# Performance work log

Hardware: AMD Instinct MI355X
Metric: run time of the kernel (lower is better)

The kernel has to match this reference:

```python
import jax, jax.numpy as jnp
import numpy as np

D_MODEL = 1024


def setup_inputs() -> dict:
    key = jax.random.key(0)
    ks = jax.random.split(key, 11)
    B, Sq, Skv, D = 16, 2048, 2048, D_MODEL
    s = 1.0 / np.sqrt(D)
    return {
        "q": jax.random.normal(ks[0], (B, Sq, D), jnp.float32),
        "k": jax.random.normal(ks[1], (B, Skv, D), jnp.float32),
        "v": jax.random.normal(ks[2], (B, Skv, D), jnp.float32),
        "Wq": jax.random.normal(ks[3], (D, D), jnp.float32) * s,
        "bq": jnp.zeros((D,), jnp.float32),
        "Wk": jax.random.normal(ks[4], (D, D), jnp.float32) * s,
        "bk": jnp.zeros((D,), jnp.float32),
        "Wv": jax.random.normal(ks[5], (D, D), jnp.float32) * s,
        "bv": jnp.zeros((D,), jnp.float32),
        "Wo": jax.random.normal(ks[6], (D, D), jnp.float32) * s,
        "bo": jnp.zeros((D,), jnp.float32),
    }


def reference(q, k, v, Wq, bq, Wk, bk, Wv, bv, Wo, bo):
    D = q.shape[-1]
    # Projections (torch Linear: x @ W^T + b; here W stored as [in, out])
    query = q @ Wq + bq          # [B, Sq, D]
    key_p = k @ Wk + bk          # [B, Skv, D]
    value = v @ Wv + bv          # [B, Skv, D]
    # Scaled dot-product attention, scale by sqrt(d_model) (single head)
    scores = jnp.einsum('bqd,bkd->bqk', query / jnp.sqrt(jnp.float32(D)), key_p)
    attn = jax.nn.softmax(scores, axis=-1)   # dropout p=0.0 -> identity
    out = jnp.einsum('bqk,bkd->bqd', attn, value)
    return out @ Wo + bo
```

## Files before the change

### kernel.cpp

```cpp
#include <hip/hip_runtime.h>

typedef unsigned int u32;
typedef unsigned short u16;
typedef __attribute__((ext_vector_type(8))) __bf16 bf16x8;
typedef __attribute__((ext_vector_type(4))) float f32x4;

typedef __attribute__((address_space(1))) void as1_void;
typedef __attribute__((address_space(3))) void as3_void;

__device__ __forceinline__ u16 f2bf(float f){
  u32 u = __builtin_bit_cast(u32, f);
  return (u16)((u + 0x7FFFu + ((u >> 16) & 1u)) >> 16);
}
__device__ __forceinline__ float bf2f(u16 h){
  u32 u = ((u32)h) << 16;
  return __builtin_bit_cast(float, u);
}

__device__ __forceinline__ void gload16(const void* g, void* l){
  __builtin_amdgcn_global_load_lds((as1_void*)(unsigned long long)g, (as3_void*)l, 16, 0, 0);
}
__device__ __forceinline__ bf16x8 ldfrag(const char* p){
  return __builtin_bit_cast(bf16x8, *(const uint4*)p);
}

__global__ void wcast(const float* __restrict__ W, float scale, u16* __restrict__ out){
  __shared__ float t[32][33];
  int bx = blockIdx.x * 32, by = blockIdx.y * 32;
  int tx = threadIdx.x, ty = threadIdx.y;
  #pragma unroll
  for (int i = 0; i < 32; i += 8) t[ty + i][tx] = W[(size_t)(bx + ty + i) * 1024 + by + tx];
  __syncthreads();
  #pragma unroll
  for (int i = 0; i < 32; i += 8)
    out[(size_t)(by + ty + i) * 1024 + bx + tx] = f2bf(scale * t[tx][ty + i]);
}

__global__ __launch_bounds__(256) void castbf(const float* __restrict__ in, u16* __restrict__ out, int n8){
  int stride = gridDim.x * blockDim.x;
  for (int i = blockIdx.x * blockDim.x + threadIdx.x; i < n8; i += stride){
    const float4* p = (const float4*)(in + (size_t)i * 8);
    float4 f0 = p[0], f1 = p[1];
    union { uint4 u; u16 h[8]; } uu;
    uu.h[0]=f2bf(f0.x); uu.h[1]=f2bf(f0.y); uu.h[2]=f2bf(f0.z); uu.h[3]=f2bf(f0.w);
    uu.h[4]=f2bf(f1.x); uu.h[5]=f2bf(f1.y); uu.h[6]=f2bf(f1.z); uu.h[7]=f2bf(f1.w);
    ((uint4*)out)[i] = uu.u;
  }
}

__global__ __launch_bounds__(256) void softmax_rows(u16* __restrict__ S){
  __shared__ float red[8];
  size_t row = blockIdx.x;
  uint4* p = (uint4*)(S + row * 2048);
  int tid = threadIdx.x;
  int lane = tid & 63, wave = tid >> 6;
  union { uint4 u4; u16 h[8]; } uu;
  uu.u4 = p[tid];
  float v[8];
  float m = -1e30f;
  #pragma unroll
  for (int j = 0; j < 8; j++){ v[j] = bf2f(uu.h[j]); m = fmaxf(m, v[j]); }
  #pragma unroll
  for (int o = 32; o; o >>= 1) m = fmaxf(m, __shfl_xor(m, o));
  if (lane == 0) red[wave] = m;
  __syncthreads();
  m = fmaxf(fmaxf(red[0], red[1]), fmaxf(red[2], red[3]));
  float s = 0.f;
  #pragma unroll
  for (int j = 0; j < 8; j++){ v[j] = __expf(v[j] - m); s += v[j]; }
  #pragma unroll
  for (int o = 32; o; o >>= 1) s += __shfl_xor(s, o);
  if (lane == 0) red[4 + wave] = s;
  __syncthreads();
  s = red[4] + red[5] + red[6] + red[7];
  float inv = 1.f / s;
  #pragma unroll
  for (int j = 0; j < 8; j++) uu.h[j] = f2bf(v[j] * inv);
  p[tid] = uu.u4;
}


template<int MO, int N0>
__device__ __forceinline__ void phase_mfma(f32x4 (&acc)[8][4], bf16x8 (&a)[4][2], bf16x8 (&b)[4][2]){
  __builtin_amdgcn_s_setprio(1);
  #pragma unroll
  for (int ks = 0; ks < 2; ks++)
    #pragma unroll
    for (int mm = 0; mm < 4; mm++)
      #pragma unroll
      for (int nn = 0; nn < 2; nn++)
        acc[MO + mm][N0 + nn] = __builtin_amdgcn_mfma_f32_16x16x32_bf16(
            a[mm][ks], b[N0 + nn][ks], acc[MO + mm][N0 + nn], 0, 0, 0);
  __builtin_amdgcn_s_setprio(0);
}

template<int BIAS, int OUTF32>
__global__ __launch_bounds__(512, 2) void gemm8(
    const u16* __restrict__ A, const u16* __restrict__ B, void* __restrict__ C,
    const float* __restrict__ bias, float bscale, int K,
    long long sA, long long sB, long long sC,
    int lda, int ldb, int ldc, int gx, int gxy)
{
  __shared__ u16 sm[2][2][16384];
  char* smb = (char*)&sm[0][0][0];

  int tid = threadIdx.x;
  int lane = tid & 63, wave = tid >> 6;
  int wr = wave >> 2, wc = wave & 3;
  int l15 = lane & 15, l4 = lane >> 4;

  int nwg = gxy * gridDim.z;
  int lin = blockIdx.x + gx * blockIdx.y + gxy * blockIdx.z;
  int cpx = nwg >> 3;
  int swz = (lin & 7) * cpx + (lin >> 3);
  int tz = swz / gxy; int rem = swz - tz * gxy;
  int ty = rem / gx;  int tx = rem - ty * gx;
  long long zb = tz;
  int row0 = tx * 256, col0 = ty * 256;

  const char* Aglob = (const char*)(A + zb * sA + (size_t)row0 * lda);
  const char* Bglob = (const char*)(B + zb * sB + (size_t)col0 * ldb);

  int r = tid >> 3, cl = tid & 7;
  int ldsb = r * 128 + cl * 16;
  u32 aoff[4], boff[4];
  #pragma unroll
  for (int i = 0; i < 4; i++){
    int row = i * 64 + r;
    int ksw = (cl ^ (r & 7)) * 8;
    aoff[i] = (u32)(((u32)row * (u32)lda + (u32)ksw) * 2u);
    boff[i] = (u32)(((u32)row * (u32)ldb + (u32)ksw) * 2u);
  }
  u32 ardo[2], brdo[2];
  #pragma unroll
  for (int ks = 0; ks < 2; ks++){
    u32 sw = (u32)(((ks * 4 + l4) ^ (l15 & 7)) * 16);
    ardo[ks] = (u32)(wr * 16384 + l15 * 128) + sw;
    brdo[ks] = (u32)(wc * 8192 + l15 * 128) + sw;
  }

#define STA(i, tau, bb) gload16(Aglob + aoff[i] + (size_t)(tau) * 128, smb + (bb) * 65536 + (i) * 8192 + ldsb)
#define STB(i, tau, bb) gload16(Bglob + boff[i] + (size_t)(tau) * 128, smb + (bb) * 65536 + 32768 + (i) * 8192 + ldsb)

  int NT = K >> 6;

  STA(0, 0, 0); STA(2, 0, 0);
  STB(0, 0, 0); STB(1, 0, 0);
  STB(2, 0, 0); STB(3, 0, 0);
  STA(1, 0, 0); STA(3, 0, 0);
  STA(0, 1, 1); STA(2, 1, 1);
  STB(0, 1, 1); STB(1, 1, 1);
  STB(2, 1, 1); STB(3, 1, 1);
  asm volatile("s_waitcnt vmcnt(6)" ::: "memory");
  __builtin_amdgcn_s_barrier();

  f32x4 acc[8][4] = {};
  bf16x8 a[4][2], b[4][2];

  for (int t = 0; t < NT; t++){
    int cur = t & 1;
    const char* Abase = smb + cur * 65536;
    const char* Bbase = Abase + 32768;

    #pragma unroll
    for (int mm = 0; mm < 4; mm++)
      #pragma unroll
      for (int ks = 0; ks < 2; ks++)
        a[mm][ks] = ldfrag(Abase + mm * 2048 + ardo[ks]);
    #pragma unroll
    for (int nn = 0; nn < 2; nn++)
      #pragma unroll
      for (int ks = 0; ks < 2; ks++)
        b[nn][ks] = ldfrag(Bbase + nn * 2048 + brdo[ks]);
    if (t + 1 < NT){ STA(1, t + 1, cur ^ 1); STA(3, t + 1, cur ^ 1); }
    __builtin_amdgcn_s_barrier();
    phase_mfma<0, 0>(acc, a, b);
    __builtin_amdgcn_s_barrier();

    #pragma unroll
    for (int nn = 2; nn < 4; nn++)
      #pragma unroll
      for (int ks = 0; ks < 2; ks++)
        b[nn][ks] = ldfrag(Bbase + nn * 2048 + brdo[ks]);
    if (t + 2 < NT){ STA(0, t + 2, cur); STA(2, t + 2, cur); }
    __builtin_amdgcn_s_barrier();
    phase_mfma<0, 2>(acc, a, b);
    __builtin_amdgcn_s_barrier();

    #pragma unroll
    for (int mm = 0; mm < 4; mm++)
      #pragma unroll
      for (int ks = 0; ks < 2; ks++)
        a[mm][ks] = ldfrag(Abase + (4 + mm) * 2048 + ardo[ks]);
    if (t + 2 < NT){ STB(0, t + 2, cur); STB(1, t + 2, cur); }
    __builtin_amdgcn_s_barrier();
    phase_mfma<4, 0>(acc, a, b);
    __builtin_amdgcn_s_barrier();

    if (t + 2 < NT){ STB(2, t + 2, cur); STB(3, t + 2, cur); }
    if (t < NT - 2) asm volatile("s_waitcnt vmcnt(6)" ::: "memory");
    else            asm volatile("s_waitcnt vmcnt(0)" ::: "memory");
    __builtin_amdgcn_s_barrier();
    phase_mfma<4, 2>(acc, a, b);
    __builtin_amdgcn_s_barrier();
  }
#undef STA
#undef STB

  #pragma unroll
  for (int m = 0; m < 8; m++){
    #pragma unroll
    for (int n = 0; n < 4; n++){
      int gr0 = row0 + wr * 128 + m * 16 + l4 * 4;
      int gc  = col0 + wc * 64 + n * 16 + l15;
      float bcol = (BIAS == 1) ? bscale * bias[gc] : 0.f;
      #pragma unroll
      for (int j = 0; j < 4; j++){
        float vv = acc[m][n][j];
        int gr = gr0 + j;
        if (BIAS == 1) vv += bcol;
        if (BIAS == 2) vv += bscale * bias[gr];
        if (OUTF32) ((float*)C)[zb * sC + (size_t)gr * ldc + gc] = vv;
        else        ((u16*) C)[zb * sC + (size_t)gr * ldc + gc] = f2bf(vv);
      }
    }
  }
}

extern "C" void kernel_launch(void* const* d_in, const int* in_sizes, int n_in,
                              void* d_out, int out_size, void* d_ws, size_t ws_size,
                              hipStream_t stream){
  const float* q  = (const float*)d_in[0];
  const float* k  = (const float*)d_in[1];
  const float* v  = (const float*)d_in[2];
  const float* Wq = (const float*)d_in[3];
  const float* bq = (const float*)d_in[4];
  const float* Wk = (const float*)d_in[5];
  const float* bk = (const float*)d_in[6];
  const float* Wv = (const float*)d_in[7];
  const float* bv = (const float*)d_in[8];
  const float* Wo = (const float*)d_in[9];
  const float* bo = (const float*)d_in[10];

  char* ws = (char*)d_ws;
  const size_t MB = (size_t)1 << 20;
  u16* Wqt = (u16*)(ws + 0 * MB);
  u16* Wkt = (u16*)(ws + 2 * MB);
  u16* Wvt = (u16*)(ws + 4 * MB);
  u16* Wot = (u16*)(ws + 6 * MB);
  u16* Qp  = (u16*)(ws + 8 * MB);
  u16* Kp  = (u16*)(ws + 72 * MB);
  u16* Vt  = (u16*)(ws + 136 * MB);
  u16* S   = (u16*)(ws + 200 * MB);
  u16* O   = (u16*)(ws + 328 * MB);
  u16* X   = (u16*)(ws + 200 * MB);
  float* out = (float*)d_out;

  dim3 wb(32, 8);
  wcast<<<dim3(32, 32), wb, 0, stream>>>(Wq, 1.f / 32.f, Wqt);
  wcast<<<dim3(32, 32), wb, 0, stream>>>(Wk, 1.f, Wkt);
  wcast<<<dim3(32, 32), wb, 0, stream>>>(Wv, 1.f, Wvt);
  wcast<<<dim3(32, 32), wb, 0, stream>>>(Wo, 1.f, Wot);

  const int n8 = 16 * 2048 * 1024 / 8;

  castbf<<<dim3(2048), 256, 0, stream>>>(q, X, n8);
  gemm8<1,0><<<dim3(128, 4, 1), 512, 0, stream>>>(X, Wqt, Qp, bq, 1.f/32.f,
      1024, 0, 0, 0, 1024, 1024, 1024, 128, 512);
  castbf<<<dim3(2048), 256, 0, stream>>>(k, X, n8);
  gemm8<1,0><<<dim3(128, 4, 1), 512, 0, stream>>>(X, Wkt, Kp, bk, 1.f,
      1024, 0, 0, 0, 1024, 1024, 1024, 128, 512);
  castbf<<<dim3(2048), 256, 0, stream>>>(v, X, n8);
  gemm8<2,0><<<dim3(4, 8, 16), 512, 0, stream>>>(Wvt, X, Vt, bv, 1.f,
      1024, 0, 2048LL * 1024, 1024LL * 2048, 1024, 1024, 2048, 4, 32);
  gemm8<0,0><<<dim3(8, 8, 16), 512, 0, stream>>>(Qp, Kp, S, nullptr, 0.f,
      1024, 2048LL * 1024, 2048LL * 1024, 2048LL * 2048, 1024, 1024, 2048, 8, 64);
  softmax_rows<<<dim3(32768), 256, 0, stream>>>(S);
  gemm8<0,0><<<dim3(8, 4, 16), 512, 0, stream>>>(S, Vt, O, nullptr, 0.f,
      2048, 2048LL * 2048, 1024LL * 2048, 2048LL * 1024, 2048, 2048, 1024, 8, 32);
  gemm8<1,1><<<dim3(128, 4, 1), 512, 0, stream>>>(O, Wot, out, bo, 1.f,
      1024, 0, 0, 0, 1024, 1024, 1024, 128, 512);
}
```

Measured before the change: 727.3 us.

## Make GEMM persistent over multiple tiles with cross-tile prefetch pipelining

The GEMM kernel now launches a fixed 256 workgroups, each processing TPB consecutive output tiles. The global-to-LDS prefetch pipeline continues across tile boundaries, so the ramp-up and drain of the double buffer overlap with the next tile and the tail wave is removed. The value bias is moved from the V projection, where it was a row bias, into the attention-times-V GEMM as a column bias. This relies on softmax rows summing to one. The tile-to-workgroup mapping assumes tile counts are multiples of 256*TPB, which adds complexity and register pressure.

```diff
diff --git a/kernel.cpp b/kernel.cpp
--- a/kernel.cpp
+++ b/kernel.cpp
@@ -97,29 +97,20 @@
 template<int BIAS, int OUTF32>
 __global__ __launch_bounds__(512, 2) void gemm8(
     const u16* __restrict__ A, const u16* __restrict__ B, void* __restrict__ C,
-    const float* __restrict__ bias, float bscale, int K,
+    const float* __restrict__ bias, float bscale, int NT,
     long long sA, long long sB, long long sC,
-    int lda, int ldb, int ldc, int gx, int gxy)
+    int lda, int ldb, int ldc, int gx, int gxy, int TPB)
 {
   __shared__ u16 sm[2][2][16384];
-  char* smb = (char*)&sm[0][0][0];
+  char* smb = (char*)sm;
 
   int tid = threadIdx.x;
   int lane = tid & 63, wave = tid >> 6;
   int wr = wave >> 2, wc = wave & 3;
   int l15 = lane & 15, l4 = lane >> 4;
 
-  int nwg = gxy * gridDim.z;
-  int lin = blockIdx.x + gx * blockIdx.y + gxy * blockIdx.z;
-  int cpx = nwg >> 3;
-  int swz = (lin & 7) * cpx + (lin >> 3);
-  int tz = swz / gxy; int rem = swz - tz * gxy;
-  int ty = rem / gx;  int tx = rem - ty * gx;
-  long long zb = tz;
-  int row0 = tx * 256, col0 = ty * 256;
-
-  const char* Aglob = (const char*)(A + zb * sA + (size_t)row0 * lda);
-  const char* Bglob = (const char*)(B + zb * sB + (size_t)col0 * ldb);
+  int b = blockIdx.x;
+  int lin0 = ((b & 7) * 32 + (b >> 3)) * TPB;
 
   int r = tid >> 3, cl = tid & 7;
   int ldsb = r * 128 + cl * 16;
@@ -139,92 +130,129 @@
     brdo[ks] = (u32)(wc * 8192 + l15 * 128) + sw;
   }
 
-#define STA(i, tau, bb) gload16(Aglob + aoff[i] + (size_t)(tau) * 128, smb + (bb) * 65536 + (i) * 8192 + ldsb)
-#define STB(i, tau, bb) gload16(Bglob + boff[i] + (size_t)(tau) * 128, smb + (bb) * 65536 + 32768 + (i) * 8192 + ldsb)
-
-  int NT = K >> 6;
-
-  STA(0, 0, 0); STA(2, 0, 0);
-  STB(0, 0, 0); STB(1, 0, 0);
-  STB(2, 0, 0); STB(3, 0, 0);
-  STA(1, 0, 0); STA(3, 0, 0);
-  STA(0, 1, 1); STA(2, 1, 1);
-  STB(0, 1, 1); STB(1, 1, 1);
-  STB(2, 1, 1); STB(3, 1, 1);
+  auto tcoord = [&](int lin, int& x, int& y, int& z){
+    z = lin / gxy; int rem = lin - z * gxy; y = rem / gx; x = rem - y * gx;
+  };
+  auto abase = [&](int lin){ int x, y, z; tcoord(lin, x, y, z);
+    return (const char*)(A + (long long)z * sA + (size_t)(x * 256) * lda); };
+  auto bbase = [&](int lin){ int x, y, z; tcoord(lin, x, y, z);
+    return (const char*)(B + (long long)z * sB + (size_t)(y * 256) * ldb); };
+
+  int tx, ty, tz;
+  tcoord(lin0, tx, ty, tz);
+  int row0 = tx * 256, col0 = ty * 256;
+  long long zbC = tz;
+
+  float bc0[4], bc1[4];
+  if (BIAS){
+    int xx, yy, zz;
+    tcoord(lin0, xx, yy, zz);
+    int c0 = yy * 256 + wc * 64 + l15;
+    #pragma unroll
+    for (int n = 0; n < 4; n++) bc0[n] = bscale * bias[c0 + n * 16];
+    tcoord(lin0 + (TPB > 1 ? 1 : 0), xx, yy, zz);
+    c0 = yy * 256 + wc * 64 + l15;
+    #pragma unroll
+    for (int n = 0; n < 4; n++) bc1[n] = bscale * bias[c0 + n * 16];
+  }
+
+  const char* AgM = abase(lin0);
+  const char* AgP = AgM;
+  const char* BgP = bbase(lin0);
+  int km = 1, kp = 2, jm = 0, jp = 0, kk = 0, jj = 0;
+
+#define STA(bse, i, kq, bb) gload16((bse) + aoff[i] + (size_t)(kq) * 128, smb + (bb) * 65536 + (i) * 8192 + ldsb)
+#define STB(bse, i, kq, bb) gload16((bse) + boff[i] + (size_t)(kq) * 128, smb + (bb) * 65536 + 32768 + (i) * 8192 + ldsb)
+
+  STA(AgM, 0, 0, 0); STA(AgM, 2, 0, 0);
+  STB(BgP, 0, 0, 0); STB(BgP, 1, 0, 0); STB(BgP, 2, 0, 0); STB(BgP, 3, 0, 0);
+  STA(AgM, 1, 0, 0); STA(AgM, 3, 0, 0);
+  STA(AgM, 0, 1, 1); STA(AgM, 2, 1, 1);
+  STB(BgP, 0, 1, 1); STB(BgP, 1, 1, 1); STB(BgP, 2, 1, 1); STB(BgP, 3, 1, 1);
   asm volatile("s_waitcnt vmcnt(6)" ::: "memory");
   __builtin_amdgcn_s_barrier();
 
   f32x4 acc[8][4] = {};
-  bf16x8 a[4][2], b[4][2];
-
-  for (int t = 0; t < NT; t++){
-    int cur = t & 1;
-    const char* Abase = smb + cur * 65536;
-    const char* Bbase = Abase + 32768;
+  bf16x8 a[4][2], bfr[4][2];
+  int S = TPB * NT;
+
+  for (int s = 0; s < S; s++){
+    int cur = s & 1;
+    const char* Ab = smb + cur * 65536;
+    const char* Bb = Ab + 32768;
+    bool st1 = (s + 1 < S), st2 = (s + 2 < S);
 
     #pragma unroll
     for (int mm = 0; mm < 4; mm++)
       #pragma unroll
       for (int ks = 0; ks < 2; ks++)
-        a[mm][ks] = ldfrag(Abase + mm * 2048 + ardo[ks]);
+        a[mm][ks] = ldfrag(Ab + mm * 2048 + ardo[ks]);
     #pragma unroll
     for (int nn = 0; nn < 2; nn++)
       #pragma unroll
       for (int ks = 0; ks < 2; ks++)
-        b[nn][ks] = ldfrag(Bbase + nn * 2048 + brdo[ks]);
-    if (t + 1 < NT){ STA(1, t + 1, cur ^ 1); STA(3, t + 1, cur ^ 1); }
-    __builtin_amdgcn_s_barrier();
-    phase_mfma<0, 0>(acc, a, b);
+        bfr[nn][ks] = ldfrag(Bb + nn * 2048 + brdo[ks]);
+    if (st1){ STA(AgM, 1, km, cur ^ 1); STA(AgM, 3, km, cur ^ 1); }
+    __builtin_amdgcn_s_barrier();
+    phase_mfma<0, 0>(acc, a, bfr);
     __builtin_amdgcn_s_barrier();
 
     #pragma unroll
     for (int nn = 2; nn < 4; nn++)
       #pragma unroll
       for (int ks = 0; ks < 2; ks++)
-        b[nn][ks] = ldfrag(Bbase + nn * 2048 + brdo[ks]);
-    if (t + 2 < NT){ STA(0, t + 2, cur); STA(2, t + 2, cur); }
-    __builtin_amdgcn_s_barrier();
-    phase_mfma<0, 2>(acc, a, b);
+        bfr[nn][ks] = ldfrag(Bb + nn * 2048 + brdo[ks]);
+    if (st2){ STA(AgP, 0, kp, cur); STA(AgP, 2, kp, cur); }
+    __builtin_amdgcn_s_barrier();
+    phase_mfma<0, 2>(acc, a, bfr);
     __builtin_amdgcn_s_barrier();
 
     #pragma unroll
     for (int mm = 0; mm < 4; mm++)
       #pragma unroll
       for (int ks = 0; ks < 2; ks++)
-        a[mm][ks] = ldfrag(Abase + (4 + mm) * 2048 + ardo[ks]);
-    if (t + 2 < NT){ STB(0, t + 2, cur); STB(1, t + 2, cur); }
-    __builtin_amdgcn_s_barrier();
-    phase_mfma<4, 0>(acc, a, b);
-    __builtin_amdgcn_s_barrier();
-
-    if (t + 2 < NT){ STB(2, t + 2, cur); STB(3, t + 2, cur); }
-    if (t < NT - 2) asm volatile("s_waitcnt vmcnt(6)" ::: "memory");
-    else            asm volatile("s_waitcnt vmcnt(0)" ::: "memory");
-    __builtin_amdgcn_s_barrier();
-    phase_mfma<4, 2>(acc, a, b);
-    __builtin_amdgcn_s_barrier();
+        a[mm][ks] = ldfrag(Ab + (4 + mm) * 2048 + ardo[ks]);
+    if (st2){ STB(BgP, 0, kp, cur); STB(BgP, 1, kp, cur); }
+    __builtin_amdgcn_s_barrier();
+    phase_mfma<4, 0>(acc, a, bfr);
+    __builtin_amdgcn_s_barrier();
+
+    if (st2){ STB(BgP, 2, kp, cur); STB(BgP, 3, kp, cur); }
+    if (s < S - 2) asm volatile("s_waitcnt vmcnt(6)" ::: "memory");
+    else           asm volatile("s_waitcnt vmcnt(0)" ::: "memory");
+    __builtin_amdgcn_s_barrier();
+    phase_mfma<4, 2>(acc, a, bfr);
+    __builtin_amdgcn_s_barrier();
+
+    if (++km == NT){ km = 0; if (++jm < TPB) AgM = abase(lin0 + jm); }
+    if (++kp == NT){ kp = 0; if (++jp < TPB){ AgP = abase(lin0 + jp); BgP = bbase(lin0 + jp); } }
+    if (++kk == NT){
+      kk = 0;
+      #pragma unroll
+      for (int m = 0; m < 8; m++){
+        #pragma unroll
+        for (int n = 0; n < 4; n++){
+          int gr0 = row0 + wr * 128 + m * 16 + l4 * 4;
+          int gc  = col0 + wc * 64 + n * 16 + l15;
+          float bcol = BIAS ? (jj == 0 ? bc0[n] : bc1[n]) : 0.f;
+          #pragma unroll
+          for (int j = 0; j < 4; j++){
+            float vv = acc[m][n][j] + bcol;
+            int gr = gr0 + j;
+            if (OUTF32) ((float*)C)[zbC * sC + (size_t)gr * ldc + gc] = vv;
+            else        ((u16*) C)[zbC * sC + (size_t)gr * ldc + gc] = f2bf(vv);
+          }
+          acc[m][n] = (f32x4){0.f, 0.f, 0.f, 0.f};
+        }
+      }
+      if (++jj < TPB){
+        tcoord(lin0 + jj, tx, ty, tz);
+        row0 = tx * 256; col0 = ty * 256; zbC = tz;
+      }
+    }
   }
 #undef STA
 #undef STB
-
-  #pragma unroll
-  for (int m = 0; m < 8; m++){
-    #pragma unroll
-    for (int n = 0; n < 4; n++){
-      int gr0 = row0 + wr * 128 + m * 16 + l4 * 4;
-      int gc  = col0 + wc * 64 + n * 16 + l15;
-      float bcol = (BIAS == 1) ? bscale * bias[gc] : 0.f;
-      #pragma unroll
-      for (int j = 0; j < 4; j++){
-        float vv = acc[m][n][j];
-        int gr = gr0 + j;
-        if (BIAS == 1) vv += bcol;
-        if (BIAS == 2) vv += bscale * bias[gr];
-        if (OUTF32) ((float*)C)[zb * sC + (size_t)gr * ldc + gc] = vv;
-        else        ((u16*) C)[zb * sC + (size_t)gr * ldc + gc] = f2bf(vv);
-      }
-    }
-  }
 }
 
 extern "C" void kernel_launch(void* const* d_in, const int* in_sizes, int n_in,
@@ -265,19 +293,19 @@
   const int n8 = 16 * 2048 * 1024 / 8;
 
   castbf<<<dim3(2048), 256, 0, stream>>>(q, X, n8);
-  gemm8<1,0><<<dim3(128, 4, 1), 512, 0, stream>>>(X, Wqt, Qp, bq, 1.f/32.f,
-      1024, 0, 0, 0, 1024, 1024, 1024, 128, 512);
+  gemm8<1,0><<<dim3(256), 512, 0, stream>>>(X, Wqt, Qp, bq, 1.f/32.f,
+      16, 0, 0, 0, 1024, 1024, 1024, 128, 512, 2);
   castbf<<<dim3(2048), 256, 0, stream>>>(k, X, n8);
-  gemm8<1,0><<<dim3(128, 4, 1), 512, 0, stream>>>(X, Wkt, Kp, bk, 1.f,
-      1024, 0, 0, 0, 1024, 1024, 1024, 128, 512);
+  gemm8<1,0><<<dim3(256), 512, 0, stream>>>(X, Wkt, Kp, bk, 1.f,
+      16, 0, 0, 0, 1024, 1024, 1024, 128, 512, 2);
   castbf<<<dim3(2048), 256, 0, stream>>>(v, X, n8);
-  gemm8<2,0><<<dim3(4, 8, 16), 512, 0, stream>>>(Wvt, X, Vt, bv, 1.f,
-      1024, 0, 2048LL * 1024, 1024LL * 2048, 1024, 1024, 2048, 4, 32);
-  gemm8<0,0><<<dim3(8, 8, 16), 512, 0, stream>>>(Qp, Kp, S, nullptr, 0.f,
-      1024, 2048LL * 1024, 2048LL * 1024, 2048LL * 2048, 1024, 1024, 2048, 8, 64);
+  gemm8<0,0><<<dim3(256), 512, 0, stream>>>(Wvt, X, Vt, nullptr, 0.f,
+      16, 0, 2048LL * 1024, 1024LL * 2048, 1024, 1024, 2048, 4, 32, 2);
+  gemm8<0,0><<<dim3(256), 512, 0, stream>>>(Qp, Kp, S, nullptr, 0.f,
+      16, 2048LL * 1024, 2048LL * 1024, 2048LL * 2048, 1024, 1024, 2048, 8, 64, 4);
   softmax_rows<<<dim3(32768), 256, 0, stream>>>(S);
-  gemm8<0,0><<<dim3(8, 4, 16), 512, 0, stream>>>(S, Vt, O, nullptr, 0.f,
-      2048, 2048LL * 2048, 1024LL * 2048, 2048LL * 1024, 2048, 2048, 1024, 8, 32);
-  gemm8<1,1><<<dim3(128, 4, 1), 512, 0, stream>>>(O, Wot, out, bo, 1.f,
-      1024, 0, 0, 0, 1024, 1024, 1024, 128, 512);
-}
+  gemm8<1,0><<<dim3(256), 512, 0, stream>>>(S, Vt, O, bv, 1.f,
+      32, 2048LL * 2048, 1024LL * 2048, 2048LL * 1024, 2048, 2048, 1024, 8, 32, 2);
+  gemm8<1,1><<<dim3(256), 512, 0, stream>>>(O, Wot, out, bo, 1.f,
+      16, 0, 0, 0, 1024, 1024, 1024, 128, 512, 2);
+}
```

Measured after the change: 728.2 us. No clear change (+0.1%).
